# Kernel tuning notes

Hardware: AMD Instinct MI355X
Metric: run time of the kernel (lower is better)

Reference implementation:

```python
import jax, jax.numpy as jnp
import numpy as np

NUM_Q_HEADS = 32
NUM_KV_HEADS = 8
HEAD_DIM = 128
ROPE_THETA = 10000.0
Q_SIZE = NUM_Q_HEADS * HEAD_DIM      # 4096
KV_SIZE = NUM_KV_HEADS * HEAD_DIM    # 1024


def _apply_rope_neox(x, positions, theta=ROPE_THETA):
    # x: [T, H, D]; neox-style rotate-halves RoPE
    T, H, D = x.shape
    half = D // 2
    inv_freq = 1.0 / (theta ** (jnp.arange(half, dtype=jnp.float32) / half))
    freqs = positions.astype(jnp.float32)[:, None] * inv_freq[None, :]  # [T, half]
    cos = jnp.cos(freqs)[:, None, :]  # [T, 1, half]
    sin = jnp.sin(freqs)[:, None, :]
    x1, x2 = x[..., :half], x[..., half:]
    return jnp.concatenate([x1 * cos - x2 * sin, x2 * cos + x1 * sin], axis=-1).astype(x.dtype)


def setup_inputs() -> dict:
    key = jax.random.key(0)
    k1, k2, k3 = jax.random.split(key, 3)
    T, E = 8192, 4096
    hidden_states = jax.random.normal(k1, (T, E), dtype=jnp.float32) * 0.02
    positions = jnp.arange(T, dtype=jnp.int32)
    w_qkv = jax.random.normal(k2, (E, Q_SIZE + 2 * KV_SIZE), dtype=jnp.float32) * 0.02
    w_o = jax.random.normal(k3, (Q_SIZE, E), dtype=jnp.float32) * 0.02
    return {"hidden_states": hidden_states, "positions": positions, "w_qkv": w_qkv, "w_o": w_o}


def reference(hidden_states, positions, w_qkv, w_o):
    T = hidden_states.shape[0]
    qkv = hidden_states @ w_qkv                              # [T, 6144]
    q = qkv[:, :Q_SIZE].reshape(T, NUM_Q_HEADS, HEAD_DIM)
    k = qkv[:, Q_SIZE:Q_SIZE + KV_SIZE].reshape(T, NUM_KV_HEADS, HEAD_DIM)
    v = qkv[:, Q_SIZE + KV_SIZE:]                            # [T, KV_SIZE] (unused by stub)
    q = _apply_rope_neox(q, positions)
    k = _apply_rope_neox(k, positions)
    # Attention is stubbed in the source (randn_like(q)); we use the RoPE'd q
    # as the deterministic stand-in so the pipeline stays reproducible.
    attn_output = q.reshape(T, Q_SIZE)
    output = attn_output @ w_o                               # [T, 4096]
    return output
```

## Files before the change

kernel.cpp:

```cpp
#include <hip/hip_runtime.h>
#include <hip/hip_bf16.h>
#include <stdint.h>

#define T_DIM 8192
#define E_DIM 4096
#define NQH   32
#define HD    128
#define QSZ   (NQH * HD)
#define QKV_COLS 6144

typedef unsigned short u16;
typedef __attribute__((ext_vector_type(8))) short   bf16x8;
typedef __attribute__((ext_vector_type(4))) float   f32x4;
typedef __attribute__((ext_vector_type(4))) unsigned short u16x4;

__device__ __forceinline__ u16 f2bf(float f) {
    uint32_t u = __float_as_uint(f);
    u += 0x7fffu + ((u >> 16) & 1u);
    return (u16)(u >> 16);
}
__device__ __forceinline__ float bf2f(u16 u) {
    return __uint_as_float(((uint32_t)u) << 16);
}

__device__ __forceinline__ void gload_lds16(u16* lds, const u16* g) {
    __builtin_amdgcn_global_load_lds(
        (const __attribute__((address_space(1))) uint32_t*)g,
        (__attribute__((address_space(3))) uint32_t*)lds,
        16, 0, 0);
}

__global__ void convert_f32_bf16(const float* __restrict__ in, u16* __restrict__ out, size_t n4) {
    size_t i = (size_t)blockIdx.x * blockDim.x + threadIdx.x;
    size_t stride = (size_t)gridDim.x * blockDim.x;
    for (; i < n4; i += stride) {
        float4 v = ((const float4*)in)[i];
        u16x4 o;
        o.x = f2bf(v.x); o.y = f2bf(v.y); o.z = f2bf(v.z); o.w = f2bf(v.w);
        ((u16x4*)out)[i] = o;
    }
}

__global__ void transpose_conv(const float* __restrict__ W, u16* __restrict__ Wt,
                               int K, int N, int ldW, int colOff) {
    __shared__ float tile[32][33];
    const int tx = threadIdx.x, ty = threadIdx.y;
    const int n0 = blockIdx.x * 32, k0 = blockIdx.y * 32;
#pragma unroll
    for (int j = 0; j < 4; ++j) {
        int k = k0 + ty + j * 8;
        tile[ty + j * 8][tx] = W[(size_t)k * ldW + colOff + n0 + tx];
    }
    __syncthreads();
#pragma unroll
    for (int j = 0; j < 4; ++j) {
        int n = n0 + ty + j * 8;
        Wt[(size_t)n * K + k0 + tx] = f2bf(tile[tx][ty + j * 8]);
    }
}

__global__ void rope_kernel(u16* __restrict__ Q, const int* __restrict__ pos) {
    const size_t total = (size_t)T_DIM * (QSZ / 2);
    size_t stride = (size_t)gridDim.x * blockDim.x;
    for (size_t idx = (size_t)blockIdx.x * blockDim.x + threadIdx.x; idx < total; idx += stride) {
        int t = (int)(idx >> 11);
        int r = (int)(idx & 2047);
        int h = r >> 6;
        int d = r & 63;
        size_t base = (size_t)t * QSZ + h * HD;
        float x1 = bf2f(Q[base + d]);
        float x2 = bf2f(Q[base + d + 64]);
        float inv = powf(10000.0f, -(float)d * (1.0f / 64.0f));
        float fr  = (float)pos[t] * inv;
        float s, c;
        sincosf(fr, &s, &c);
        Q[base + d]      = f2bf(x1 * c - x2 * s);
        Q[base + d + 64] = f2bf(x2 * c + x1 * s);
    }
}

__device__ __forceinline__ void store_out(u16* p, float v)  { *p = f2bf(v); }
__device__ __forceinline__ void store_out(float* p, float v){ *p = v; }

#define BAR() do { __builtin_amdgcn_sched_barrier(0); __builtin_amdgcn_s_barrier(); \
                   __builtin_amdgcn_sched_barrier(0); } while (0)
#define VMC(N) asm volatile("s_waitcnt vmcnt(%0)" :: "n"(N) : "memory")

#define STG_A(buf, h, kOff) do { \
    const u16* s_ = sA + (size_t)(h) * 128 * K + (kOff); \
    u16* d_ = dL + (buf) * 32768 + (h) * 8192; \
    gload_lds16(d_, s_); gload_lds16(d_ + 4096, s_ + (size_t)64 * K); } while (0)
#define STG_B(buf, h, kOff) do { \
    const u16* s_ = sB + (size_t)(h) * 128 * K + (kOff); \
    u16* d_ = dL + 16384 + (buf) * 32768 + (h) * 8192; \
    gload_lds16(d_, s_); gload_lds16(d_ + 4096, s_ + (size_t)64 * K); } while (0)

#define RD_A(buf, miBase) do { _Pragma("unroll") \
    for (int m = 0; m < 4; ++m) { \
        const u16* p_ = lds + (buf) * 32768 + wm * 8192 + ((miBase) + m) * 1024 + aRow; \
        aK0[m] = *(const bf16x8*)(p_ + cOf0); \
        aK1[m] = *(const bf16x8*)(p_ + cOf1); } } while (0)
#define RD_B(buf, niBase, d0, d1) do { _Pragma("unroll") \
    for (int n = 0; n < 2; ++n) { \
        const u16* p_ = lds + (buf) * 32768 + 16384 + (wn >> 1) * 8192 + \
                        ((wn & 1) * 64 + ((niBase) + n) * 16) * 64 + aRow; \
        d0[n] = *(const bf16x8*)(p_ + cOf0); \
        d1[n] = *(const bf16x8*)(p_ + cOf1); } } while (0)

#define MM(miBase, niBase, bq0, bq1) do { \
    __builtin_amdgcn_s_setprio(1); \
    _Pragma("unroll") for (int m = 0; m < 4; ++m) \
    _Pragma("unroll") for (int n = 0; n < 2; ++n) { \
        acc[(miBase) + m][(niBase) + n] = __builtin_amdgcn_mfma_f32_16x16x32_bf16( \
            aK0[m], bq0[n], acc[(miBase) + m][(niBase) + n], 0, 0, 0); \
        acc[(miBase) + m][(niBase) + n] = __builtin_amdgcn_mfma_f32_16x16x32_bf16( \
            aK1[m], bq1[n], acc[(miBase) + m][(niBase) + n], 0, 0, 0); } \
    __builtin_amdgcn_s_setprio(0); } while (0)

template <typename OutT>
__global__ __launch_bounds__(512, 2) void gemm256(const u16* __restrict__ A,
                                                  const u16* __restrict__ Bt,
                                                  OutT* __restrict__ C,
                                                  int M, int N, int K) {
    __shared__ u16 lds[65536];
    const int tid  = threadIdx.x;
    const int lane = tid & 63;
    const int wid  = tid >> 6;
    const int wm = wid >> 2;
    const int wn = wid & 3;
    const int lr  = lane & 15;
    const int kq  = lane >> 4;
    const int lr7 = lr & 7;
    const int aRow = lr * 64;
    const int cOf0 = ((kq) ^ lr7) << 3;
    const int cOf1 = ((4 + kq) ^ lr7) << 3;

    const int nwg = gridDim.x;
    const int cpx = nwg >> 3;
    const int bid = blockIdx.x;
    const int swz = (bid & 7) * cpx + (bid >> 3);
    const int numM = M >> 8;
    const size_t rowBase = (size_t)(swz % numM) << 8;
    const size_t colBase = (size_t)(swz / numM) << 8;

    const int r0 = tid >> 3;
    const int cS = (((tid & 7) ^ (r0 & 7)) << 3);
    const u16* sA = A  + (rowBase + r0) * (size_t)K + cS;
    const u16* sB = Bt + (colBase + r0) * (size_t)K + cS;
    u16* dL = &lds[0] + tid * 8;

    f32x4 acc[8][4];
#pragma unroll
    for (int i = 0; i < 8; ++i)
#pragma unroll
        for (int j = 0; j < 4; ++j)
            acc[i][j] = (f32x4){0.f, 0.f, 0.f, 0.f};

    bf16x8 aK0[4], aK1[4], b01K0[2], b01K1[2], b23K0[2], b23K1[2];

    STG_A(0, 0, 0); STG_A(0, 1, 0); STG_B(0, 0, 0); STG_B(0, 1, 0);
    STG_B(1, 0, 64); STG_B(1, 1, 64);
    VMC(4);
    BAR();

    const int nIter = K >> 7;
    for (int it = 0; it < nIter; ++it) {
        const int k1  = ((it << 1) + 1) << 6;
        const int kt2 = ((it << 1) + 2) << 6;
        const int kt3 = ((it << 1) + 3) << 6;
        const int k2c = (kt2 <= K - 64) ? kt2 : 0;
        const int k3c = (kt3 <= K - 64) ? kt3 : 0;

        RD_A(0, 0); RD_B(0, 0, b01K0, b01K1);
        STG_A(1, 0, k1);
        BAR();
        MM(0, 0, b01K0, b01K1);
        BAR();
        RD_B(0, 2, b23K0, b23K1);
        STG_A(1, 1, k1);
        BAR();
        MM(0, 2, b23K0, b23K1);
        BAR();
        RD_A(0, 4);
        STG_B(0, 0, k2c);
        BAR();
        MM(4, 2, b23K0, b23K1);
        BAR();
        STG_B(0, 1, k2c);
        VMC(4);
        BAR();
        MM(4, 0, b01K0, b01K1);
        BAR();
        RD_A(1, 0); RD_B(1, 0, b01K0, b01K1);
        STG_A(0, 0, k2c);
        BAR();
        MM(0, 0, b01K0, b01K1);
        BAR();
        RD_B(1, 2, b23K0, b23K1);
        STG_A(0, 1, k2c);
        BAR();
        MM(0, 2, b23K0, b23K1);
        BAR();
        RD_A(1, 4);
        STG_B(1, 0, k3c);
        BAR();
        MM(4, 2, b23K0, b23K1);
        BAR();
        STG_B(1, 1, k3c);
        VMC(4);
        BAR();
        MM(4, 0, b01K0, b01K1);
        BAR();
    }

    asm volatile("s_waitcnt vmcnt(0)" ::: "memory");

#pragma unroll
    for (int mi = 0; mi < 8; ++mi)
#pragma unroll
        for (int ni = 0; ni < 4; ++ni)
#pragma unroll
            for (int r = 0; r < 4; ++r) {
                size_t row = rowBase + wm * 128 + mi * 16 + (kq << 2) + r;
                size_t col = colBase + wn * 64 + ni * 16 + lr;
                store_out(&C[row * (size_t)N + col], acc[mi][ni][r]);
            }
}

extern "C" void kernel_launch(void* const* d_in, const int* in_sizes, int n_in,
                              void* d_out, int out_size, void* d_ws, size_t ws_size,
                              hipStream_t stream) {
    const float* hidden    = (const float*)d_in[0];
    const int*   positions = (const int*)d_in[1];
    const float* w_qkv     = (const float*)d_in[2];
    const float* w_o       = (const float*)d_in[3];
    float* out = (float*)d_out;

    u16* Hb  = (u16*)d_ws;
    u16* WqT = Hb  + (size_t)T_DIM * E_DIM;
    u16* WoT = WqT + (size_t)QSZ * E_DIM;
    u16* Qb  = WoT + (size_t)E_DIM * QSZ;

    convert_f32_bf16<<<2048, 256, 0, stream>>>(hidden, Hb, (size_t)T_DIM * E_DIM / 4);

    dim3 tb(32, 8);
    transpose_conv<<<dim3(QSZ / 32, E_DIM / 32), tb, 0, stream>>>(w_qkv, WqT, E_DIM, QSZ, QKV_COLS, 0);
    transpose_conv<<<dim3(E_DIM / 32, QSZ / 32), tb, 0, stream>>>(w_o,   WoT, QSZ,   E_DIM, E_DIM,  0);

    gemm256<u16><<<dim3((T_DIM / 256) * (QSZ / 256)), 512, 0, stream>>>(Hb, WqT, Qb, T_DIM, QSZ, E_DIM);

    rope_kernel<<<4096, 256, 0, stream>>>(Qb, positions);

    gemm256<float><<<dim3((T_DIM / 256) * (E_DIM / 256)), 512, 0, stream>>>(Qb, WoT, out, T_DIM, E_DIM, QSZ);
}
```

Before: 615.9 us.

## Double-buffer MFMA operand registers and interleave LDS reads with MFMA

Splits the A and B fragment registers into separate sets (a0/a4, even/odd b01) so the LDS reads for the next sub-tile are issued alongside the MFMAs of the current one. This halves the number of workgroup barriers per K step. It also prefetches the first fragments before the loop and at the end of each iteration. The aim is to hide LDS read latency behind matrix math and cut barrier stalls, at the cost of more VGPRs and a more delicate ordering of LDS reads against the async global-to-LDS writes.

```diff
diff --git a/kernel.cpp b/kernel.cpp
--- a/kernel.cpp
+++ b/kernel.cpp
@@ -82,8 +82,9 @@
 __device__ __forceinline__ void store_out(u16* p, float v)  { *p = f2bf(v); }
 __device__ __forceinline__ void store_out(float* p, float v){ *p = v; }
 
-#define BAR() do { __builtin_amdgcn_sched_barrier(0); __builtin_amdgcn_s_barrier(); \
-                   __builtin_amdgcn_sched_barrier(0); } while (0)
+#define BARS()    do { __builtin_amdgcn_sched_barrier(0); __builtin_amdgcn_s_barrier(); } while (0)
+#define BARSPUB() do { __builtin_amdgcn_sched_barrier(0); __builtin_amdgcn_s_barrier(); \
+                       __builtin_amdgcn_sched_barrier(0); } while (0)
 #define VMC(N) asm volatile("s_waitcnt vmcnt(%0)" :: "n"(N) : "memory")
 
 #define STG_A(buf, h, kOff) do { \
@@ -95,11 +96,11 @@
     u16* d_ = dL + 16384 + (buf) * 32768 + (h) * 8192; \
     gload_lds16(d_, s_); gload_lds16(d_ + 4096, s_ + (size_t)64 * K); } while (0)
 
-#define RD_A(buf, miBase) do { _Pragma("unroll") \
+#define RD_A(buf, miBase, d0, d1) do { _Pragma("unroll") \
     for (int m = 0; m < 4; ++m) { \
         const u16* p_ = lds + (buf) * 32768 + wm * 8192 + ((miBase) + m) * 1024 + aRow; \
-        aK0[m] = *(const bf16x8*)(p_ + cOf0); \
-        aK1[m] = *(const bf16x8*)(p_ + cOf1); } } while (0)
+        d0[m] = *(const bf16x8*)(p_ + cOf0); \
+        d1[m] = *(const bf16x8*)(p_ + cOf1); } } while (0)
 #define RD_B(buf, niBase, d0, d1) do { _Pragma("unroll") \
     for (int n = 0; n < 2; ++n) { \
         const u16* p_ = lds + (buf) * 32768 + 16384 + (wn >> 1) * 8192 + \
@@ -107,14 +108,14 @@
         d0[n] = *(const bf16x8*)(p_ + cOf0); \
         d1[n] = *(const bf16x8*)(p_ + cOf1); } } while (0)
 
-#define MM(miBase, niBase, bq0, bq1) do { \
+#define MM(miBase, niBase, A0, A1, B0, B1) do { \
     __builtin_amdgcn_s_setprio(1); \
     _Pragma("unroll") for (int m = 0; m < 4; ++m) \
     _Pragma("unroll") for (int n = 0; n < 2; ++n) { \
         acc[(miBase) + m][(niBase) + n] = __builtin_amdgcn_mfma_f32_16x16x32_bf16( \
-            aK0[m], bq0[n], acc[(miBase) + m][(niBase) + n], 0, 0, 0); \
+            A0[m], B0[n], acc[(miBase) + m][(niBase) + n], 0, 0, 0); \
         acc[(miBase) + m][(niBase) + n] = __builtin_amdgcn_mfma_f32_16x16x32_bf16( \
-            aK1[m], bq1[n], acc[(miBase) + m][(niBase) + n], 0, 0, 0); } \
+            A1[m], B1[n], acc[(miBase) + m][(niBase) + n], 0, 0, 0); } \
     __builtin_amdgcn_s_setprio(0); } while (0)
 
 template <typename OutT>
@@ -156,12 +157,15 @@
         for (int j = 0; j < 4; ++j)
             acc[i][j] = (f32x4){0.f, 0.f, 0.f, 0.f};
 
-    bf16x8 aK0[4], aK1[4], b01K0[2], b01K1[2], b23K0[2], b23K1[2];
+    bf16x8 a0K0[4], a0K1[4], a4K0[4], a4K1[4];
+    bf16x8 b01eK0[2], b01eK1[2], b01oK0[2], b01oK1[2], b23K0[2], b23K1[2];
 
     STG_A(0, 0, 0); STG_A(0, 1, 0); STG_B(0, 0, 0); STG_B(0, 1, 0);
     STG_B(1, 0, 64); STG_B(1, 1, 64);
     VMC(4);
-    BAR();
+    BARSPUB();
+    RD_A(0, 0, a0K0, a0K1);
+    RD_B(0, 0, b01eK0, b01eK1);
 
     const int nIter = K >> 7;
     for (int it = 0; it < nIter; ++it) {
@@ -171,46 +175,40 @@
         const int k2c = (kt2 <= K - 64) ? kt2 : 0;
         const int k3c = (kt3 <= K - 64) ? kt3 : 0;
 
-        RD_A(0, 0); RD_B(0, 0, b01K0, b01K1);
         STG_A(1, 0, k1);
-        BAR();
-        MM(0, 0, b01K0, b01K1);
-        BAR();
+        BARS();
         RD_B(0, 2, b23K0, b23K1);
+        MM(0, 0, a0K0, a0K1, b01eK0, b01eK1);
         STG_A(1, 1, k1);
-        BAR();
-        MM(0, 2, b23K0, b23K1);
-        BAR();
-        RD_A(0, 4);
+        BARS();
+        RD_A(0, 4, a4K0, a4K1);
+        MM(0, 2, a0K0, a0K1, b23K0, b23K1);
         STG_B(0, 0, k2c);
-        BAR();
-        MM(4, 2, b23K0, b23K1);
-        BAR();
+        BARS();
+        MM(4, 2, a4K0, a4K1, b23K0, b23K1);
         STG_B(0, 1, k2c);
         VMC(4);
-        BAR();
-        MM(4, 0, b01K0, b01K1);
-        BAR();
-        RD_A(1, 0); RD_B(1, 0, b01K0, b01K1);
+        BARSPUB();
+        RD_A(1, 0, a0K0, a0K1);
+        RD_B(1, 0, b01oK0, b01oK1);
+        MM(4, 0, a4K0, a4K1, b01eK0, b01eK1);
         STG_A(0, 0, k2c);
-        BAR();
-        MM(0, 0, b01K0, b01K1);
-        BAR();
+        BARS();
         RD_B(1, 2, b23K0, b23K1);
+        MM(0, 0, a0K0, a0K1, b01oK0, b01oK1);
         STG_A(0, 1, k2c);
-        BAR();
-        MM(0, 2, b23K0, b23K1);
-        BAR();
-        RD_A(1, 4);
+        BARS();
+        RD_A(1, 4, a4K0, a4K1);
+        MM(0, 2, a0K0, a0K1, b23K0, b23K1);
         STG_B(1, 0, k3c);
-        BAR();
-        MM(4, 2, b23K0, b23K1);
-        BAR();
+        BARS();
+        MM(4, 2, a4K0, a4K1, b23K0, b23K1);
         STG_B(1, 1, k3c);
         VMC(4);
-        BAR();
-        MM(4, 0, b01K0, b01K1);
-        BAR();
+        BARSPUB();
+        RD_A(0, 0, a0K0, a0K1);
+        RD_B(0, 0, b01eK0, b01eK1);
+        MM(4, 0, a4K0, a4K1, b01oK0, b01oK1);
     }
 
     asm volatile("s_waitcnt vmcnt(0)" ::: "memory");
```

Measured after the change: 605.7 us. Within noise of the previous version (-1.6%).
